# Kernel tuning notes

Hardware: AMD Instinct MI355X
Metric: run time of the kernel (lower is better)

Reference implementation:

```python
import jax, jax.numpy as jnp
import numpy as np

N_NODES = 200000
N_EDGES = 6400000
N_REL = 16


def rgcn_layer(x, src, dst, etype, W, root, b, num_nodes):
    # FastRGCNConv math: per-edge m_e = x[src_e] @ W[etype_e], mean-aggregated at dst,
    # plus root transform and bias. We precompute x @ W for all relations (N,R,Fout)
    # then gather per edge -- avoids materializing per-edge (Fin,Fout) weight copies.
    xW = jnp.einsum('nf,rfo->nro', x, W)          # [N, R, Fout]
    msg = xW[src, etype]                           # [E, Fout] gather
    agg = jax.ops.segment_sum(msg, dst, num_segments=num_nodes)
    deg = jax.ops.segment_sum(jnp.ones((src.shape[0],), x.dtype), dst,
                              num_segments=num_nodes)
    agg = agg / jnp.maximum(deg, 1.0)[:, None]     # mean aggregation (0 for isolated nodes)
    return agg + x @ root + b


def setup_inputs() -> dict:
    key = jax.random.key(0)
    ks = jax.random.split(key, 8)
    x = jax.random.normal(ks[0], (N_NODES, 7), dtype=jnp.float32)
    edge_index = jax.random.randint(ks[1], (2, N_EDGES), 0, N_NODES, dtype=jnp.int64)
    edge_type = jax.random.randint(ks[2], (N_EDGES,), 0, N_REL, dtype=jnp.int64)
    W1 = jax.random.normal(ks[3], (N_REL, 7, 16), dtype=jnp.float32) * 0.3
    root1 = jax.random.normal(ks[4], (7, 16), dtype=jnp.float32) * 0.3
    b1 = jnp.zeros((16,), dtype=jnp.float32)
    W2 = jax.random.normal(ks[5], (N_REL, 16, 2), dtype=jnp.float32) * 0.3
    root2 = jax.random.normal(ks[6], (16, 2), dtype=jnp.float32) * 0.3
    b2 = jnp.zeros((2,), dtype=jnp.float32)
    return {"x": x, "edge_index": edge_index, "edge_type": edge_type,
            "W1": W1, "root1": root1, "b1": b1,
            "W2": W2, "root2": root2, "b2": b2}


def reference(x, edge_index, edge_type, W1, root1, b1, W2, root2, b2):
    num_nodes = x.shape[0]
    src, dst = edge_index[0], edge_index[1]
    h = jax.nn.relu(rgcn_layer(x, src, dst, edge_type, W1, root1, b1, num_nodes))
    out = rgcn_layer(h, src, dst, edge_type, W2, root2, b2, num_nodes)
    return jax.nn.log_softmax(out, axis=1)
```

## Files before the change

### kernel.cpp

```cpp
#include <hip/hip_runtime.h>
#include <hip/hip_fp16.h>
#include <math.h>


#define BLOCK 256
#define NREL 16
#define DBIN 256
#define BKT_ST 17
#define CH   8192
#define BINS_MAX   1024
#define CHUNKS_MAX 1024
#define SCAN 1024

#define SC2  1048576.0f
#define ISC2 (1.0f/1048576.0f)
#define HQS  16.0f
#define IHQS (1.0f/16.0f)


__device__ __forceinline__ long long q8f(float v) {
    v = fminf(fmaxf(v, -14.f), 14.f);
    return (long long)(int)rintf(v * 8.0f);
}

__device__ __forceinline__ unsigned long long pack7x(const float* xp) {
    long long t = q8f(xp[0]) + (q8f(xp[1]) << 8) + (q8f(xp[2]) << 16)
                + (q8f(xp[3]) << 24) + (q8f(xp[4]) << 32) + (q8f(xp[5]) << 40)
                + (q8f(xp[6]) << 48) + (1LL << 56);
    return (unsigned long long)t;
}

__device__ __forceinline__ void unpack7x(long long t, float* f, float* cnt) {
#pragma unroll
    for (int i = 0; i < 7; ++i) {
        int fi = (int)(signed char)(t & 0xFF);
        t = (t - fi) >> 8;
        f[i] = fi * 0.125f;
    }
    *cnt = (float)(int)t;
}

__device__ __forceinline__ float2 uh2f2(unsigned u) {
    __half2 t; __builtin_memcpy(&t, &u, 4);
    return __half22float2(t);
}
__device__ __forceinline__ unsigned f2uh2(float a, float b) {
    __half2 t = __floats2half2_rn(a, b);
    unsigned u; __builtin_memcpy(&u, &t, 4);
    return u;
}


__global__ __launch_bounds__(BLOCK) void k_prep(
    const float* __restrict__ x, unsigned long long* __restrict__ qx, int N)
{
    int n = blockIdx.x * BLOCK + threadIdx.x;
    if (n < N) qx[n] = pack7x(x + (size_t)n * 7);
}


__global__ __launch_bounds__(BLOCK) void k_hist(
    const int* __restrict__ dst, unsigned* __restrict__ chunkCnt,
    unsigned* __restrict__ binTotal, unsigned* __restrict__ lofsG,
    int E, int nb)
{
    __shared__ unsigned hist[BINS_MAX];
    __shared__ unsigned wsum[BLOCK / 64];
    for (int i = threadIdx.x; i < nb; i += BLOCK) hist[i] = 0;
    __syncthreads();

    int c = blockIdx.x;
    int base = c * CH;
    const int4* dst4 = (const int4*)(dst + base);
#pragma unroll
    for (int k = 0; k < CH / (BLOCK * 4); ++k) {
        int item = k * BLOCK + threadIdx.x;
        int e0 = base + item * 4;
        if (e0 + 3 < E) {
            int4 d = dst4[item];
            atomicAdd(&hist[(unsigned)d.x >> 8], 1u);
            atomicAdd(&hist[(unsigned)d.y >> 8], 1u);
            atomicAdd(&hist[(unsigned)d.z >> 8], 1u);
            atomicAdd(&hist[(unsigned)d.w >> 8], 1u);
        } else {
#pragma unroll
            for (int j = 0; j < 4; ++j) {
                int e = e0 + j;
                if (e < E) atomicAdd(&hist[(unsigned)dst[e] >> 8], 1u);
            }
        }
    }
    __syncthreads();

    for (int i = threadIdx.x; i < nb; i += BLOCK) {
        unsigned cn = hist[i];
        chunkCnt[(size_t)c * nb + i] = cn;
        if (cn) atomicAdd(&binTotal[i], cn);
    }

    unsigned v[4];
    unsigned tsum = 0;
#pragma unroll
    for (int j = 0; j < 4; ++j) {
        int bi = 4 * (int)threadIdx.x + j;
        v[j] = (bi < nb) ? hist[bi] : 0u;
        tsum += v[j];
    }
    int lane = threadIdx.x & 63, wid = threadIdx.x >> 6;
    unsigned inc = tsum;
#pragma unroll
    for (int ofs = 1; ofs < 64; ofs <<= 1) {
        unsigned o = (unsigned)__shfl_up((int)inc, ofs);
        if (lane >= ofs) inc += o;
    }
    if (lane == 63) wsum[wid] = inc;
    __syncthreads();
    unsigned wofs = 0;
    for (int w = 0; w < wid; ++w) wofs += wsum[w];
    unsigned run = wofs + inc - tsum;
    unsigned* lg = lofsG + (size_t)c * (nb + 1);
#pragma unroll
    for (int j = 0; j < 4; ++j) {
        int bi = 4 * (int)threadIdx.x + j;
        if (bi < nb) lg[bi] = run;
        run += v[j];
    }
    if ((int)threadIdx.x == BLOCK - 1) lg[nb] = run;
}

__global__ __launch_bounds__(BLOCK) void k_scan(
    const unsigned* __restrict__ chunkCnt, const unsigned* __restrict__ binTotal,
    unsigned* __restrict__ chunkOfs, unsigned* __restrict__ binBase,
    int nb, int nc)
{
    __shared__ unsigned sA[SCAN], sB[SCAN];
    int b = blockIdx.x;

    unsigned* cur = sA; unsigned* nxt = sB;
    for (int i = threadIdx.x; i < SCAN; i += BLOCK)
        cur[i] = (i < nb) ? binTotal[i] : 0u;
    __syncthreads();
    for (int ofs = 1; ofs < SCAN; ofs <<= 1) {
        for (int i = threadIdx.x; i < SCAN; i += BLOCK)
            nxt[i] = cur[i] + ((i >= ofs) ? cur[i - ofs] : 0u);
        __syncthreads();
        unsigned* t = cur; cur = nxt; nxt = t;
    }
    unsigned binBase_b = (b > 0) ? cur[b - 1] : 0u;
    if (threadIdx.x == 0) binBase[b] = binBase_b;
    __syncthreads();

    for (int i = threadIdx.x; i < SCAN; i += BLOCK)
        cur[i] = (i < nc) ? chunkCnt[(size_t)i * nb + b] : 0u;
    __syncthreads();
    for (int ofs = 1; ofs < SCAN; ofs <<= 1) {
        for (int i = threadIdx.x; i < SCAN; i += BLOCK)
            nxt[i] = cur[i] + ((i >= ofs) ? cur[i - ofs] : 0u);
        __syncthreads();
        unsigned* t = cur; cur = nxt; nxt = t;
    }
    for (int i = threadIdx.x; i < nc; i += BLOCK)
        chunkOfs[(size_t)i * nb + b] = binBase_b + ((i > 0) ? cur[i - 1] : 0u);
}

__global__ __launch_bounds__(BLOCK) void k_scatter3(
    const int* __restrict__ src, const int* __restrict__ dst,
    const int* __restrict__ et, const unsigned* __restrict__ lofsG,
    const unsigned* __restrict__ chunkOfs, unsigned* __restrict__ rec,
    int E, int nb)
{
    __shared__ unsigned stg[CH];
    __shared__ unsigned short lofs[BINS_MAX + 1];
    __shared__ unsigned curi[BINS_MAX];

    int c = blockIdx.x;
    const unsigned* lg = lofsG + (size_t)c * (nb + 1);
    for (int i = threadIdx.x; i <= nb; i += BLOCK) {
        unsigned l = lg[i];
        lofs[i] = (unsigned short)l;
        if (i < nb) curi[i] = l;
    }
    __syncthreads();

    int base = c * CH;
    const int4* src4 = (const int4*)(src + base);
    const int4* dst4 = (const int4*)(dst + base);
    const int4* et4  = (const int4*)(et + base);
#pragma unroll
    for (int k = 0; k < CH / (BLOCK * 4); ++k) {
        int item = k * BLOCK + threadIdx.x;
        int e0 = base + item * 4;
        if (e0 + 3 < E) {
            int4 s = src4[item], d = dst4[item], t = et4[item];
            {
                unsigned slot = atomicAdd(&curi[(unsigned)d.x >> 8], 1u);
                stg[slot] = (unsigned)s.x | ((unsigned)t.x << 18) | (((unsigned)d.x & 255u) << 22);
            }
            {
                unsigned slot = atomicAdd(&curi[(unsigned)d.y >> 8], 1u);
                stg[slot] = (unsigned)s.y | ((unsigned)t.y << 18) | (((unsigned)d.y & 255u) << 22);
            }
            {
                unsigned slot = atomicAdd(&curi[(unsigned)d.z >> 8], 1u);
                stg[slot] = (unsigned)s.z | ((unsigned)t.z << 18) | (((unsigned)d.z & 255u) << 22);
            }
            {
                unsigned slot = atomicAdd(&curi[(unsigned)d.w >> 8], 1u);
                stg[slot] = (unsigned)s.w | ((unsigned)t.w << 18) | (((unsigned)d.w & 255u) << 22);
            }
        } else {
#pragma unroll
            for (int j = 0; j < 4; ++j) {
                int e = e0 + j;
                if (e < E) {
                    unsigned d = (unsigned)dst[e];
                    unsigned slot = atomicAdd(&curi[d >> 8], 1u);
                    stg[slot] = (unsigned)src[e] | ((unsigned)et[e] << 18) | ((d & 255u) << 22);
                }
            }
        }
    }
    __syncthreads();

    int total = min(CH, E - base);
    const unsigned* cofs = chunkOfs + (size_t)c * nb;
    for (int i = threadIdx.x; i < total; i += BLOCK) {
        int lo = 0, hi = nb;
        while (hi - lo > 1) {
            int mid = (lo + hi) >> 1;
            if ((int)lofs[mid] <= i) lo = mid; else hi = mid;
        }
        rec[cofs[lo] + (unsigned)(i - (int)lofs[lo])] = stg[i];
    }
}


__global__ __launch_bounds__(BLOCK) void k_agg1(
    const float* __restrict__ x, const unsigned long long* __restrict__ qx,
    const unsigned* __restrict__ rec,
    const unsigned* __restrict__ binBase, const unsigned* __restrict__ binTotal,
    const float* __restrict__ W1, const float* __restrict__ root1,
    const float* __restrict__ b1, unsigned* __restrict__ h2,
    uint4* __restrict__ qh, float* __restrict__ deg, int N)
{
    __shared__ unsigned long long bkt[DBIN * BKT_ST];
    __shared__ float w[NREL * 112];
    __shared__ float r1[112];
    __shared__ float bb[16];

    for (int i = threadIdx.x; i < DBIN * BKT_ST; i += BLOCK) bkt[i] = 0ull;
    for (int i = threadIdx.x; i < NREL * 112; i += BLOCK) w[i] = W1[i];
    if (threadIdx.x < 112) r1[threadIdx.x] = root1[threadIdx.x];
    if (threadIdx.x < 16) bb[threadIdx.x] = b1[threadIdx.x];
    __syncthreads();

    int b = blockIdx.x;
    unsigned base = binBase[b], cnt = binTotal[b];
    for (unsigned i = threadIdx.x; i < cnt; i += BLOCK) {
        unsigned rc = rec[base + i];
        int s  = rc & 0x3FFFF;
        int r  = (rc >> 18) & 15;
        int dl = (rc >> 22) & 255;
        atomicAdd(&bkt[dl * BKT_ST + r], qx[s]);
    }
    __syncthreads();

    int dl = threadIdx.x;
    int n = b * DBIN + dl;
    if (n >= N) return;

    float acc[16];
#pragma unroll
    for (int o = 0; o < 16; ++o) acc[o] = 0.f;
    float dg = 0.f;
#pragma unroll
    for (int r = 0; r < NREL; ++r) {
        float sv[7], c;
        unpack7x((long long)bkt[dl * BKT_ST + r], sv, &c);
        dg += c;
#pragma unroll
        for (int f = 0; f < 7; ++f) {
            float xf = sv[f];
#pragma unroll
            for (int o = 0; o < 16; ++o) acc[o] += xf * w[r * 112 + f * 16 + o];
        }
    }

    float invd = 1.0f / fmaxf(dg, 1.0f);
    float xv[7];
    const float* xp = x + (size_t)n * 7;
#pragma unroll
    for (int f = 0; f < 7; ++f) xv[f] = xp[f];

    float hv[16];
#pragma unroll
    for (int oo = 0; oo < 16; ++oo) {
        float v = bb[oo] + acc[oo] * invd;
#pragma unroll
        for (int f = 0; f < 7; ++f) v += xv[f] * r1[f * 16 + oo];
        hv[oo] = fmaxf(v, 0.f);
    }
    uint4* hp = (uint4*)(h2 + ((size_t)n << 3));
    hp[0] = make_uint4(f2uh2(hv[0], hv[1]),  f2uh2(hv[2], hv[3]),
                       f2uh2(hv[4], hv[5]),  f2uh2(hv[6], hv[7]));
    hp[1] = make_uint4(f2uh2(hv[8], hv[9]),  f2uh2(hv[10], hv[11]),
                       f2uh2(hv[12], hv[13]), f2uh2(hv[14], hv[15]));

    unsigned p[4];
#pragma unroll
    for (int g = 0; g < 4; ++g) {
        unsigned v = 0;
#pragma unroll
        for (int j = 0; j < 4; ++j) {
            unsigned q = (unsigned)(int)rintf(fminf(hv[g * 4 + j], 15.9f) * HQS);
            v |= q << (8 * j);
        }
        p[g] = v;
    }
    qh[n] = make_uint4(p[0], p[1], p[2], p[3]);
    deg[n] = dg;
}

__global__ __launch_bounds__(BLOCK) void k_agg2(
    const unsigned* __restrict__ h2, const uint4* __restrict__ qh,
    const unsigned* __restrict__ rec,
    const unsigned* __restrict__ binBase, const unsigned* __restrict__ binTotal,
    const float* __restrict__ deg, const float* __restrict__ W2,
    const float* __restrict__ root2, const float* __restrict__ b2,
    float* __restrict__ out, int N)
{
    __shared__ unsigned long long a2q[DBIN];
    __shared__ float w[NREL * 32];
    __shared__ float r2[32];
    __shared__ float bb[2];

    for (int i = threadIdx.x; i < DBIN; i += BLOCK) a2q[i] = 0ull;
    for (int i = threadIdx.x; i < NREL * 32; i += BLOCK) w[i] = W2[i];
    if (threadIdx.x < 32) r2[threadIdx.x] = root2[threadIdx.x];
    if (threadIdx.x < 2) bb[threadIdx.x] = b2[threadIdx.x];
    __syncthreads();

    int b = blockIdx.x;
    unsigned base = binBase[b], cnt = binTotal[b];
    for (unsigned i = threadIdx.x; i < cnt; i += BLOCK) {
        unsigned rc = rec[base + i];
        int s  = rc & 0x3FFFF;
        int r  = (rc >> 18) & 15;
        int dl = (rc >> 22) & 255;

        uint4 q = qh[s];
        const float* wr = &w[r * 32];
        float a0 = 0.f, a1 = 0.f;
        unsigned qs[4] = {q.x, q.y, q.z, q.w};
#pragma unroll
        for (int g = 0; g < 4; ++g) {
            unsigned v = qs[g];
#pragma unroll
            for (int j = 0; j < 4; ++j) {
                float f = (float)((v >> (8 * j)) & 0xFFu) * IHQS;
                int ff = g * 4 + j;
                a0 += f * wr[ff * 2 + 0];
                a1 += f * wr[ff * 2 + 1];
            }
        }
        long long p0 = (long long)(int)rintf(a0 * SC2);
        long long p1 = (long long)(int)rintf(a1 * SC2);
        atomicAdd(&a2q[dl], (unsigned long long)(p0 + (p1 << 32)));
    }
    __syncthreads();

    int dl = threadIdx.x;
    int n = b * DBIN + dl;
    if (n >= N) return;

    float invd = 1.0f / fmaxf(deg[n], 1.0f);
    float o0 = bb[0], o1 = bb[1];
    const uint4* hp = (const uint4*)(h2 + ((size_t)n << 3));
    uint4 qa = hp[0], qb = hp[1];
    unsigned qs[8] = {qa.x, qa.y, qa.z, qa.w, qb.x, qb.y, qb.z, qb.w};
#pragma unroll
    for (int p = 0; p < 8; ++p) {
        float2 f = uh2f2(qs[p]);
        o0 += f.x * r2[(p * 2 + 0) * 2 + 0] + f.y * r2[(p * 2 + 1) * 2 + 0];
        o1 += f.x * r2[(p * 2 + 0) * 2 + 1] + f.y * r2[(p * 2 + 1) * 2 + 1];
    }
    long long t = (long long)a2q[dl];
    int q0 = (int)(t & 0xFFFFFFFFLL);
    long long t1 = (t - (long long)q0) >> 32;
    int q1 = (int)t1;
    o0 += (q0 * ISC2) * invd;
    o1 += (q1 * ISC2) * invd;

    float m = fmaxf(o0, o1);
    float lse = m + logf(expf(o0 - m) + expf(o1 - m));
    ((float2*)out)[n] = make_float2(o0 - lse, o1 - lse);
}


__global__ __launch_bounds__(BLOCK) void k_edge1e(
    const float* __restrict__ x, const int* __restrict__ src,
    const int* __restrict__ dst, const int* __restrict__ et,
    unsigned long long* __restrict__ Sq, int E)
{
    int e = blockIdx.x * BLOCK + threadIdx.x;
    if (e >= E) return;
    int s = src[e], d = dst[e], r = et[e];
    atomicAdd(Sq + (size_t)d * NREL + r, pack7x(x + (size_t)s * 7));
}

__global__ __launch_bounds__(BLOCK) void k_node1e(
    const float* __restrict__ x, const unsigned long long* __restrict__ Sq,
    const float* __restrict__ W1, const float* __restrict__ root1,
    const float* __restrict__ b1, float* __restrict__ h,
    float* __restrict__ deg, int N)
{
    __shared__ float w[NREL * 112];
    __shared__ float r1[112];
    __shared__ float bb[16];
    for (int i = threadIdx.x; i < NREL * 112; i += BLOCK) w[i] = W1[i];
    if (threadIdx.x < 112) r1[threadIdx.x] = root1[threadIdx.x];
    if (threadIdx.x < 16) bb[threadIdx.x] = b1[threadIdx.x];
    __syncthreads();

    int n = blockIdx.x * BLOCK + threadIdx.x;
    if (n >= N) return;

    float acc[16];
#pragma unroll
    for (int o = 0; o < 16; ++o) acc[o] = 0.f;
    float dg = 0.f;

    const ulonglong2* sp = (const ulonglong2*)(Sq + ((size_t)n << 4));
#pragma unroll
    for (int rp = 0; rp < NREL / 2; ++rp) {
        ulonglong2 q = sp[rp];
#pragma unroll
        for (int half = 0; half < 2; ++half) {
            int r = rp * 2 + half;
            float sv[7], c;
            unpack7x((long long)(half ? q.y : q.x), sv, &c);
            dg += c;
#pragma unroll
            for (int f = 0; f < 7; ++f) {
                float xf = sv[f];
#pragma unroll
                for (int o = 0; o < 16; ++o) acc[o] += xf * w[r * 112 + f * 16 + o];
            }
        }
    }

    float invd = 1.0f / fmaxf(dg, 1.0f);
    float xv[7];
    const float* xp = x + (size_t)n * 7;
#pragma unroll
    for (int f = 0; f < 7; ++f) xv[f] = xp[f];

    float4* hp = (float4*)(h + ((size_t)n << 4));
#pragma unroll
    for (int og = 0; og < 4; ++og) {
        float o[4];
#pragma unroll
        for (int oi = 0; oi < 4; ++oi) {
            int oo = og * 4 + oi;
            float v = bb[oo] + acc[oo] * invd;
#pragma unroll
            for (int f = 0; f < 7; ++f) v += xv[f] * r1[f * 16 + oo];
            o[oi] = fmaxf(v, 0.f);
        }
        hp[og] = make_float4(o[0], o[1], o[2], o[3]);
    }
    deg[n] = dg;
}

__global__ __launch_bounds__(BLOCK) void k_edge2d(
    const float* __restrict__ h, const int* __restrict__ src,
    const int* __restrict__ dst, const int* __restrict__ et,
    const float* __restrict__ W2, unsigned long long* __restrict__ agg2, int E)
{
    __shared__ float w[NREL * 32];
    for (int i = threadIdx.x; i < NREL * 32; i += BLOCK) w[i] = W2[i];
    __syncthreads();

    int e = blockIdx.x * BLOCK + threadIdx.x;
    if (e >= E) return;
    int s = src[e], d = dst[e], r = et[e];

    const float4* hp = (const float4*)(h + ((size_t)s << 4));
    const float* wr = &w[r * 32];
    float a0 = 0.f, a1 = 0.f;
#pragma unroll
    for (int fg = 0; fg < 4; ++fg) {
        float4 hv = hp[fg];
        a0 += hv.x * wr[(fg * 4 + 0) * 2] + hv.y * wr[(fg * 4 + 1) * 2] +
              hv.z * wr[(fg * 4 + 2) * 2] + hv.w * wr[(fg * 4 + 3) * 2];
        a1 += hv.x * wr[(fg * 4 + 0) * 2 + 1] + hv.y * wr[(fg * 4 + 1) * 2 + 1] +
              hv.z * wr[(fg * 4 + 2) * 2 + 1] + hv.w * wr[(fg * 4 + 3) * 2 + 1];
    }
    long long p0 = (long long)(int)rintf(a0 * SC2);
    long long p1 = (long long)(int)rintf(a1 * SC2);
    atomicAdd(agg2 + d, (unsigned long long)(p0 + (p1 << 32)));
}

__global__ __launch_bounds__(BLOCK) void k_outd(
    const float* __restrict__ h, const unsigned long long* __restrict__ agg2,
    const float* __restrict__ deg, const float* __restrict__ root2,
    const float* __restrict__ b2, float* __restrict__ out, int N)
{
    __shared__ float r2[32];
    __shared__ float bb[2];
    if (threadIdx.x < 32) r2[threadIdx.x] = root2[threadIdx.x];
    if (threadIdx.x < 2) bb[threadIdx.x] = b2[threadIdx.x];
    __syncthreads();

    int n = blockIdx.x * BLOCK + threadIdx.x;
    if (n >= N) return;

    float invd = 1.0f / fmaxf(deg[n], 1.0f);
    float o0 = bb[0], o1 = bb[1];
    const float4* hp = (const float4*)(h + ((size_t)n << 4));
#pragma unroll
    for (int fg = 0; fg < 4; ++fg) {
        float4 hv = hp[fg];
        o0 += hv.x * r2[(fg * 4 + 0) * 2 + 0] + hv.y * r2[(fg * 4 + 1) * 2 + 0] +
              hv.z * r2[(fg * 4 + 2) * 2 + 0] + hv.w * r2[(fg * 4 + 3) * 2 + 0];
        o1 += hv.x * r2[(fg * 4 + 0) * 2 + 1] + hv.y * r2[(fg * 4 + 1) * 2 + 1] +
              hv.z * r2[(fg * 4 + 2) * 2 + 1] + hv.w * r2[(fg * 4 + 3) * 2 + 1];
    }
    long long t = (long long)agg2[n];
    int q0 = (int)(t & 0xFFFFFFFFLL);
    long long t1 = (t - (long long)q0) >> 32;
    int q1 = (int)t1;
    o0 += (q0 * ISC2) * invd;
    o1 += (q1 * ISC2) * invd;

    float m = fmaxf(o0, o1);
    float lse = m + logf(expf(o0 - m) + expf(o1 - m));
    ((float2*)out)[n] = make_float2(o0 - lse, o1 - lse);
}


extern "C" void kernel_launch(void* const* d_in, const int* in_sizes, int n_in,
                              void* d_out, int out_size, void* d_ws, size_t ws_size,
                              hipStream_t stream)
{
    const float* x     = (const float*)d_in[0];
    const int*   ei    = (const int*)d_in[1];
    const int*   et    = (const int*)d_in[2];
    const float* W1    = (const float*)d_in[3];
    const float* root1 = (const float*)d_in[4];
    const float* b1    = (const float*)d_in[5];
    const float* W2    = (const float*)d_in[6];
    const float* root2 = (const float*)d_in[7];
    const float* b2    = (const float*)d_in[8];
    float* out = (float*)d_out;

    const int N = in_sizes[0] / 7;
    const int E = in_sizes[1] / 2;
    const int* src = ei;
    const int* dst = ei + E;

    const int nb = (N + DBIN - 1) / DBIN;
    const int nc = (E + CH - 1) / CH;

    if (nb <= BINS_MAX && nc <= CHUNKS_MAX && N <= (1 << 18) && (E % 4) == 0) {
        char* base = (char*)d_ws;
        size_t ofs = 0;
        unsigned* rec      = (unsigned*)(base + ofs); ofs += (size_t)E * 4;
        ofs = (ofs + 255) & ~(size_t)255;
        unsigned long long* qx = (unsigned long long*)(base + ofs); ofs += (size_t)N * 8;
        ofs = (ofs + 255) & ~(size_t)255;
        unsigned* chunkCnt = (unsigned*)(base + ofs); ofs += (size_t)nc * nb * 4;
        ofs = (ofs + 255) & ~(size_t)255;
        unsigned* chunkOfs = (unsigned*)(base + ofs); ofs += (size_t)nc * nb * 4;
        ofs = (ofs + 255) & ~(size_t)255;
        unsigned* lofsG    = (unsigned*)(base + ofs); ofs += (size_t)nc * (nb + 1) * 4;
        ofs = (ofs + 255) & ~(size_t)255;
        unsigned* binTotal = (unsigned*)(base + ofs); ofs += (size_t)nb * 4;
        ofs = (ofs + 255) & ~(size_t)255;
        unsigned* binBase  = (unsigned*)(base + ofs); ofs += (size_t)nb * 4;
        ofs = (ofs + 255) & ~(size_t)255;
        unsigned* h2 = (unsigned*)(base + ofs); ofs += (size_t)N * 32;
        ofs = (ofs + 255) & ~(size_t)255;
        uint4* qh = (uint4*)(base + ofs); ofs += (size_t)N * 16;
        float* deg = (float*)(base + ofs); ofs += (size_t)N * 4;

        hipMemsetAsync(binTotal, 0, (size_t)nb * 4, stream);

        int npb = (N + BLOCK - 1) / BLOCK;
        k_prep    <<<npb, BLOCK, 0, stream>>>(x, qx, N);
        k_hist    <<<nc, BLOCK, 0, stream>>>(dst, chunkCnt, binTotal, lofsG, E, nb);
        k_scan    <<<nb, BLOCK, 0, stream>>>(chunkCnt, binTotal, chunkOfs, binBase, nb, nc);
        k_scatter3<<<nc, BLOCK, 0, stream>>>(src, dst, et, lofsG, chunkOfs, rec, E, nb);
        k_agg1    <<<nb, BLOCK, 0, stream>>>(x, qx, rec, binBase, binTotal, W1, root1, b1, h2, qh, deg, N);
        k_agg2    <<<nb, BLOCK, 0, stream>>>(h2, qh, rec, binBase, binTotal, deg, W2, root2, b2, out, N);
    } else {
        int eb = (E + BLOCK - 1) / BLOCK;
        int nbk = (N + BLOCK - 1) / BLOCK;
        char* wbase = (char*)d_ws;
        size_t agg2_ofs = (size_t)N * 128;
        size_t h_ofs    = (agg2_ofs + (size_t)N * 8 + 255) & ~(size_t)255;
        size_t deg_ofs  = h_ofs + (size_t)N * 64;

        unsigned long long* Sq   = (unsigned long long*)wbase;
        unsigned long long* agg2 = (unsigned long long*)(wbase + agg2_ofs);
        float*              h    = (float*)(wbase + h_ofs);
        float*              deg  = (float*)(wbase + deg_ofs);

        hipMemsetAsync(Sq, 0, agg2_ofs + (size_t)N * 8, stream);
        k_edge1e<<<eb, BLOCK, 0, stream>>>(x, src, dst, et, Sq, E);
        k_node1e<<<nbk, BLOCK, 0, stream>>>(x, Sq, W1, root1, b1, h, deg, N);
        k_edge2d<<<eb, BLOCK, 0, stream>>>(h, src, dst, et, W2, agg2, E);
        k_outd<<<nbk, BLOCK, 0, stream>>>(h, agg2, deg, root2, b2, out, N);
    }
}
```

Before: 325.8 us.

## Halve destination bin size, XOR-swizzle shared buckets, unroll edge gathers

Destination bins shrink from 256 to 128 nodes, so the binning, scan and record packing now use shift 7, and up to 2048 bins with 8 entries per thread in the local scan. This doubles the number of aggregation blocks and shrinks per-block shared memory, which allows more resident blocks. The padded shared bucket layout is replaced by an XOR swizzle to spread bank conflicts. Both aggregation loops are unrolled by four so independent gathers from qx/qh are in flight together. The cost is that half the threads in each aggregation block sit idle during the per-node epilogue.

```diff
diff --git a/kernel.cpp b/kernel.cpp
--- a/kernel.cpp
+++ b/kernel.cpp
@@ -5,17 +5,18 @@
 
 #define BLOCK 256
 #define NREL 16
-#define DBIN 256
-#define BKT_ST 17
+#define DBIN 128
 #define CH   8192
-#define BINS_MAX   1024
+#define BINS_MAX   2048
 #define CHUNKS_MAX 1024
-#define SCAN 1024
+#define SCAN 2048
 
 #define SC2  1048576.0f
 #define ISC2 (1.0f/1048576.0f)
 #define HQS  16.0f
 #define IHQS (1.0f/16.0f)
+
+#define BKT_IDX(dl, r) (((dl) << 4) + ((r) ^ ((dl) & 15)))
 
 
 __device__ __forceinline__ long long q8f(float v) {
@@ -78,15 +79,15 @@
         int e0 = base + item * 4;
         if (e0 + 3 < E) {
             int4 d = dst4[item];
-            atomicAdd(&hist[(unsigned)d.x >> 8], 1u);
-            atomicAdd(&hist[(unsigned)d.y >> 8], 1u);
-            atomicAdd(&hist[(unsigned)d.z >> 8], 1u);
-            atomicAdd(&hist[(unsigned)d.w >> 8], 1u);
+            atomicAdd(&hist[(unsigned)d.x >> 7], 1u);
+            atomicAdd(&hist[(unsigned)d.y >> 7], 1u);
+            atomicAdd(&hist[(unsigned)d.z >> 7], 1u);
+            atomicAdd(&hist[(unsigned)d.w >> 7], 1u);
         } else {
 #pragma unroll
             for (int j = 0; j < 4; ++j) {
                 int e = e0 + j;
-                if (e < E) atomicAdd(&hist[(unsigned)dst[e] >> 8], 1u);
+                if (e < E) atomicAdd(&hist[(unsigned)dst[e] >> 7], 1u);
             }
         }
     }
@@ -98,11 +99,11 @@
         if (cn) atomicAdd(&binTotal[i], cn);
     }
 
-    unsigned v[4];
+    unsigned v[8];
     unsigned tsum = 0;
 #pragma unroll
-    for (int j = 0; j < 4; ++j) {
-        int bi = 4 * (int)threadIdx.x + j;
+    for (int j = 0; j < 8; ++j) {
+        int bi = 8 * (int)threadIdx.x + j;
         v[j] = (bi < nb) ? hist[bi] : 0u;
         tsum += v[j];
     }
@@ -120,8 +121,8 @@
     unsigned run = wofs + inc - tsum;
     unsigned* lg = lofsG + (size_t)c * (nb + 1);
 #pragma unroll
-    for (int j = 0; j < 4; ++j) {
-        int bi = 4 * (int)threadIdx.x + j;
+    for (int j = 0; j < 8; ++j) {
+        int bi = 8 * (int)threadIdx.x + j;
         if (bi < nb) lg[bi] = run;
         run += v[j];
     }
@@ -193,20 +194,20 @@
         if (e0 + 3 < E) {
             int4 s = src4[item], d = dst4[item], t = et4[item];
             {
-                unsigned slot = atomicAdd(&curi[(unsigned)d.x >> 8], 1u);
-                stg[slot] = (unsigned)s.x | ((unsigned)t.x << 18) | (((unsigned)d.x & 255u) << 22);
+                unsigned slot = atomicAdd(&curi[(unsigned)d.x >> 7], 1u);
+                stg[slot] = (unsigned)s.x | ((unsigned)t.x << 18) | (((unsigned)d.x & 127u) << 22);
             }
             {
-                unsigned slot = atomicAdd(&curi[(unsigned)d.y >> 8], 1u);
-                stg[slot] = (unsigned)s.y | ((unsigned)t.y << 18) | (((unsigned)d.y & 255u) << 22);
+                unsigned slot = atomicAdd(&curi[(unsigned)d.y >> 7], 1u);
+                stg[slot] = (unsigned)s.y | ((unsigned)t.y << 18) | (((unsigned)d.y & 127u) << 22);
             }
             {
-                unsigned slot = atomicAdd(&curi[(unsigned)d.z >> 8], 1u);
-                stg[slot] = (unsigned)s.z | ((unsigned)t.z << 18) | (((unsigned)d.z & 255u) << 22);
+                unsigned slot = atomicAdd(&curi[(unsigned)d.z >> 7], 1u);
+                stg[slot] = (unsigned)s.z | ((unsigned)t.z << 18) | (((unsigned)d.z & 127u) << 22);
             }
             {
-                unsigned slot = atomicAdd(&curi[(unsigned)d.w >> 8], 1u);
-                stg[slot] = (unsigned)s.w | ((unsigned)t.w << 18) | (((unsigned)d.w & 255u) << 22);
+                unsigned slot = atomicAdd(&curi[(unsigned)d.w >> 7], 1u);
+                stg[slot] = (unsigned)s.w | ((unsigned)t.w << 18) | (((unsigned)d.w & 127u) << 22);
             }
         } else {
 #pragma unroll
@@ -214,8 +215,8 @@
                 int e = e0 + j;
                 if (e < E) {
                     unsigned d = (unsigned)dst[e];
-                    unsigned slot = atomicAdd(&curi[d >> 8], 1u);
-                    stg[slot] = (unsigned)src[e] | ((unsigned)et[e] << 18) | ((d & 255u) << 22);
+                    unsigned slot = atomicAdd(&curi[d >> 7], 1u);
+                    stg[slot] = (unsigned)src[e] | ((unsigned)et[e] << 18) | ((d & 127u) << 22);
                 }
             }
         }
@@ -243,12 +244,12 @@
     const float* __restrict__ b1, unsigned* __restrict__ h2,
     uint4* __restrict__ qh, float* __restrict__ deg, int N)
 {
-    __shared__ unsigned long long bkt[DBIN * BKT_ST];
+    __shared__ unsigned long long bkt[DBIN * NREL];
     __shared__ float w[NREL * 112];
     __shared__ float r1[112];
     __shared__ float bb[16];
 
-    for (int i = threadIdx.x; i < DBIN * BKT_ST; i += BLOCK) bkt[i] = 0ull;
+    for (int i = threadIdx.x; i < DBIN * NREL; i += BLOCK) bkt[i] = 0ull;
     for (int i = threadIdx.x; i < NREL * 112; i += BLOCK) w[i] = W1[i];
     if (threadIdx.x < 112) r1[threadIdx.x] = root1[threadIdx.x];
     if (threadIdx.x < 16) bb[threadIdx.x] = b1[threadIdx.x];
@@ -256,16 +257,29 @@
 
     int b = blockIdx.x;
     unsigned base = binBase[b], cnt = binTotal[b];
-    for (unsigned i = threadIdx.x; i < cnt; i += BLOCK) {
-        unsigned rc = rec[base + i];
-        int s  = rc & 0x3FFFF;
-        int r  = (rc >> 18) & 15;
-        int dl = (rc >> 22) & 255;
-        atomicAdd(&bkt[dl * BKT_ST + r], qx[s]);
+    unsigned i = base + threadIdx.x, end = base + cnt;
+    for (; i + 3u * BLOCK < end; i += 4u * BLOCK) {
+        unsigned rc0 = rec[i];
+        unsigned rc1 = rec[i + BLOCK];
+        unsigned rc2 = rec[i + 2u * BLOCK];
+        unsigned rc3 = rec[i + 3u * BLOCK];
+        unsigned long long q0 = qx[rc0 & 0x3FFFF];
+        unsigned long long q1 = qx[rc1 & 0x3FFFF];
+        unsigned long long q2 = qx[rc2 & 0x3FFFF];
+        unsigned long long q3 = qx[rc3 & 0x3FFFF];
+        atomicAdd(&bkt[BKT_IDX((rc0 >> 22) & 127, (rc0 >> 18) & 15)], q0);
+        atomicAdd(&bkt[BKT_IDX((rc1 >> 22) & 127, (rc1 >> 18) & 15)], q1);
+        atomicAdd(&bkt[BKT_IDX((rc2 >> 22) & 127, (rc2 >> 18) & 15)], q2);
+        atomicAdd(&bkt[BKT_IDX((rc3 >> 22) & 127, (rc3 >> 18) & 15)], q3);
+    }
+    for (; i < end; i += BLOCK) {
+        unsigned rc = rec[i];
+        atomicAdd(&bkt[BKT_IDX((rc >> 22) & 127, (rc >> 18) & 15)], qx[rc & 0x3FFFF]);
     }
     __syncthreads();
 
     int dl = threadIdx.x;
+    if (dl >= DBIN) return;
     int n = b * DBIN + dl;
     if (n >= N) return;
 
@@ -276,7 +290,7 @@
 #pragma unroll
     for (int r = 0; r < NREL; ++r) {
         float sv[7], c;
-        unpack7x((long long)bkt[dl * BKT_ST + r], sv, &c);
+        unpack7x((long long)bkt[BKT_IDX(dl, r)], sv, &c);
         dg += c;
 #pragma unroll
         for (int f = 0; f < 7; ++f) {
@@ -319,6 +333,31 @@
     }
     qh[n] = make_uint4(p[0], p[1], p[2], p[3]);
     deg[n] = dg;
+}
+
+__device__ __forceinline__ void agg2_edge(
+    unsigned rc, const uint4 q, const float* __restrict__ w,
+    unsigned long long* __restrict__ a2q)
+{
+    int r  = (rc >> 18) & 15;
+    int dl = (rc >> 22) & 127;
+    const float* wr = &w[r * 32];
+    float a0 = 0.f, a1 = 0.f;
+    unsigned qs[4] = {q.x, q.y, q.z, q.w};
+#pragma unroll
+    for (int g = 0; g < 4; ++g) {
+        unsigned v = qs[g];
+#pragma unroll
+        for (int j = 0; j < 4; ++j) {
+            float f = (float)((v >> (8 * j)) & 0xFFu) * IHQS;
+            int ff = g * 4 + j;
+            a0 += f * wr[ff * 2 + 0];
+            a1 += f * wr[ff * 2 + 1];
+        }
+    }
+    long long p0 = (long long)(int)rintf(a0 * SC2);
+    long long p1 = (long long)(int)rintf(a1 * SC2);
+    atomicAdd(&a2q[dl], (unsigned long long)(p0 + (p1 << 32)));
 }
 
 __global__ __launch_bounds__(BLOCK) void k_agg2(
@@ -342,34 +381,29 @@
 
     int b = blockIdx.x;
     unsigned base = binBase[b], cnt = binTotal[b];
-    for (unsigned i = threadIdx.x; i < cnt; i += BLOCK) {
-        unsigned rc = rec[base + i];
-        int s  = rc & 0x3FFFF;
-        int r  = (rc >> 18) & 15;
-        int dl = (rc >> 22) & 255;
-
-        uint4 q = qh[s];
-        const float* wr = &w[r * 32];
-        float a0 = 0.f, a1 = 0.f;
-        unsigned qs[4] = {q.x, q.y, q.z, q.w};
-#pragma unroll
-        for (int g = 0; g < 4; ++g) {
-            unsigned v = qs[g];
-#pragma unroll
-            for (int j = 0; j < 4; ++j) {
-                float f = (float)((v >> (8 * j)) & 0xFFu) * IHQS;
-                int ff = g * 4 + j;
-                a0 += f * wr[ff * 2 + 0];
-                a1 += f * wr[ff * 2 + 1];
-            }
-        }
-        long long p0 = (long long)(int)rintf(a0 * SC2);
-        long long p1 = (long long)(int)rintf(a1 * SC2);
-        atomicAdd(&a2q[dl], (unsigned long long)(p0 + (p1 << 32)));
+    unsigned i = base + threadIdx.x, end = base + cnt;
+    for (; i + 3u * BLOCK < end; i += 4u * BLOCK) {
+        unsigned rc0 = rec[i];
+        unsigned rc1 = rec[i + BLOCK];
+        unsigned rc2 = rec[i + 2u * BLOCK];
+        unsigned rc3 = rec[i + 3u * BLOCK];
+        uint4 q0 = qh[rc0 & 0x3FFFF];
+        uint4 q1 = qh[rc1 & 0x3FFFF];
+        uint4 q2 = qh[rc2 & 0x3FFFF];
+        uint4 q3 = qh[rc3 & 0x3FFFF];
+        agg2_edge(rc0, q0, w, a2q);
+        agg2_edge(rc1, q1, w, a2q);
+        agg2_edge(rc2, q2, w, a2q);
+        agg2_edge(rc3, q3, w, a2q);
+    }
+    for (; i < end; i += BLOCK) {
+        unsigned rc = rec[i];
+        agg2_edge(rc, qh[rc & 0x3FFFF], w, a2q);
     }
     __syncthreads();
 
     int dl = threadIdx.x;
+    if (dl >= DBIN) return;
     int n = b * DBIN + dl;
     if (n >= N) return;
 
```

After: 341.8 us. 1.05x slower.
